# Kernel optimization log

Hardware: AMD Instinct MI355X
Metric: run time of the kernel (lower is better)

The kernel has to match this reference:

```python
import jax, jax.numpy as jnp
import numpy as np

B, NUM_ENT, NEI, NUM_REL, S, D, TOPK = 256, 100000, 128, 5000, 32, 128, 64


def setup_inputs() -> dict:
    key = jax.random.key(0)
    ks = jax.random.split(key, 9)
    return {
        "query_head": jax.random.randint(ks[0], (B,), 0, NUM_ENT, dtype=jnp.int32),
        "edge_matrix": jax.random.randint(ks[1], (NUM_ENT, NEI, 2), 0, NUM_REL, dtype=jnp.int32),
        "support_rel_all": jax.random.randint(ks[2], (S,), 0, NUM_REL, dtype=jnp.int32),
        "cos_rel_all": jax.random.normal(ks[3], (NUM_REL, NUM_REL), dtype=jnp.float32),
        "rel_emb": jax.random.normal(ks[4], (NUM_REL, D), dtype=jnp.float32) * 0.02,
        "W_ih": jax.random.normal(ks[5], (3 * D, D), dtype=jnp.float32) * 0.05,
        "W_hh": jax.random.normal(ks[6], (3 * D, D), dtype=jnp.float32) * 0.05,
        "b_ih": jax.random.normal(ks[7], (3 * D,), dtype=jnp.float32) * 0.05,
        "b_hh": jax.random.normal(ks[8], (3 * D,), dtype=jnp.float32) * 0.05,
    }


def gru_cell(x, h, W_ih, W_hh, b_ih, b_hh):
    # torch.nn.GRUCell math. x, h: [..., D]
    gi = x @ W_ih.T + b_ih
    gh = h @ W_hh.T + b_hh
    i_r, i_z, i_n = jnp.split(gi, 3, axis=-1)
    h_r, h_z, h_n = jnp.split(gh, 3, axis=-1)
    r = jax.nn.sigmoid(i_r + h_r)
    z = jax.nn.sigmoid(i_z + h_z)
    n = jnp.tanh(i_n + r * h_n)
    return (1.0 - z) * n + z * h


def reference(query_head, edge_matrix, support_rel_all, cos_rel_all, rel_emb,
              W_ih, W_hh, b_ih, b_hh):
    b = query_head.shape[0]
    nei = edge_matrix.shape[1]
    d = rel_emb.shape[1]
    sub = cos_rel_all[support_rel_all]  # [S, num_rel]

    def expand(cur):  # cur: [b, C] int entity ids
        cand = edge_matrix[cur]                       # [b, C, nei, 2]
        cand_ent, cand_rel = cand[..., 0], cand[..., 1]
        # max over support relations of cos similarity: [b, C, nei]
        score = jnp.max(sub[:, cand_rel], axis=0)
        flat = score.reshape(b, -1)                   # [b, C*nei]
        k = min(TOPK, flat.shape[-1])
        _, idx = jax.lax.top_k(flat, k)               # [b, k]
        parent = idx // nei                           # [b, k]
        aim_ent = jnp.take_along_axis(cand_ent.reshape(b, -1), idx, axis=1)
        aim_rel = jnp.take_along_axis(cand_rel.reshape(b, -1), idx, axis=1)
        return aim_ent, aim_rel, parent

    # step 1 (root -> level 1), hidden starts at zero
    e1, r1, _ = expand(query_head[:, None])
    k = e1.shape[1]
    h1 = gru_cell(rel_emb[r1], jnp.zeros((b, k, d), rel_emb.dtype), W_ih, W_hh, b_ih, b_hh)

    # step 2
    e2, r2, p2 = expand(e1)
    parent_emb2 = jnp.take_along_axis(h1, p2[..., None], axis=1)
    parent_node2 = jnp.take_along_axis(e1, p2, axis=1)
    rel1_at2 = jnp.take_along_axis(r1, p2, axis=1)
    h2 = gru_cell(rel_emb[r2], parent_emb2, W_ih, W_hh, b_ih, b_hh)

    # step 3
    e3, r3, p3 = expand(e2)
    parent_emb3 = jnp.take_along_axis(h2, p3[..., None], axis=1)
    parent_node3 = jnp.take_along_axis(e2, p3, axis=1)
    rel2_at3 = jnp.take_along_axis(r2, p3, axis=1)
    h3 = gru_cell(rel_emb[r3], parent_emb3, W_ih, W_hh, b_ih, b_hh)

    f32 = jnp.float32
    tree_node = jnp.stack([e1, e2, e3], axis=1)                    # [b, 3, k]
    tree_emb_all = jnp.stack([h1, h2, h3], axis=1)                 # [b, 3, k, d]
    parent_index = jnp.stack(
        [p2.astype(f32), p3.astype(f32),
         jnp.broadcast_to(jnp.arange(k, dtype=f32), (b, k))], axis=1)
    parent_node = jnp.stack(
        [jnp.broadcast_to(query_head[:, None], (b, k)), parent_node2, parent_node3], axis=1)
    aim_rel_all = jnp.stack([rel1_at2, rel2_at3, r3], axis=1)
    return tree_node, tree_emb_all, parent_index, parent_node, aim_rel_all
```

## Files before the change

### kernel.cpp

```cpp
#include <hip/hip_runtime.h>
#include <hip/hip_bf16.h>

#define NEI     128
#define NUM_REL 5000
#define NSUP    32
#define D       128
#define K_TOP   64
#define NB      256
#define ROWSZ   (K_TOP * D)

#define TN_OFF  0
#define TE_OFF  49152
#define PI_OFF  6340608
#define PN_OFF  6389760
#define AR_OFF  6438912

#define SENT 0xFFFFFFFFu

typedef __hip_bfloat16 bf16;
__device__ __forceinline__ float frbf(bf16 b) { return __bfloat162float(b); }
__device__ __forceinline__ float b2f(unsigned short u) {
    unsigned x = ((unsigned)u) << 16;
    return __uint_as_float(x);
}
__device__ __forceinline__ unsigned umin2(unsigned a, unsigned b) { return a < b ? a : b; }

__device__ __forceinline__ float ldin(const void* p, size_t idx, bool isbf) {
    return isbf ? frbf(((const bf16*)p)[idx]) : ((const float*)p)[idx];
}

__device__ __forceinline__ void detect_bf16(const void* probe, int tid, int* s_flag) {
    if (tid < 64) {
        unsigned w = ((const unsigned*)probe)[tid];
        unsigned e = (w >> 7) & 0xFFu;
        unsigned long long m = __ballot(e >= 100 && e <= 135);
        if (tid == 0) *s_flag = (__popcll(m) >= 48) ? 1 : 0;
    }
    __syncthreads();
}

__device__ __forceinline__ void gemm_8x8(const float* hs, const void* W,
                                         bool isbf, int gi_, int gj,
                                         float acc[8][8]) {
    if (!isbf) {
        const float* Wf = (const float*)W;
        #pragma unroll 2
        for (int kt = 0; kt < D; kt += 4) {
            float4 hv[8], wv[8];
            #pragma unroll
            for (int n = 0; n < 8; n++)
                wv[n] = *(const float4*)&Wf[(size_t)(gj + 48 * n) * D + kt];
            #pragma unroll
            for (int m = 0; m < 8; m++)
                hv[m] = *(const float4*)&hs[(gi_ + 8 * m) * 132 + kt];
            #pragma unroll
            for (int m = 0; m < 8; m++)
                #pragma unroll
                for (int n = 0; n < 8; n++)
                    acc[m][n] += hv[m].x * wv[n].x + hv[m].y * wv[n].y
                               + hv[m].z * wv[n].z + hv[m].w * wv[n].w;
        }
    } else {
        const ushort* Wb = (const ushort*)W;
        #pragma unroll 2
        for (int kt = 0; kt < D; kt += 4) {
            float4 hv[8], wv[8];
            #pragma unroll
            for (int n = 0; n < 8; n++) {
                ushort4 t = *(const ushort4*)&Wb[(size_t)(gj + 48 * n) * D + kt];
                wv[n].x = b2f(t.x); wv[n].y = b2f(t.y);
                wv[n].z = b2f(t.z); wv[n].w = b2f(t.w);
            }
            #pragma unroll
            for (int m = 0; m < 8; m++)
                hv[m] = *(const float4*)&hs[(gi_ + 8 * m) * 132 + kt];
            #pragma unroll
            for (int m = 0; m < 8; m++)
                #pragma unroll
                for (int n = 0; n < 8; n++)
                    acc[m][n] += hv[m].x * wv[n].x + hv[m].y * wv[n].y
                               + hv[m].z * wv[n].z + hv[m].w * wv[n].w;
        }
    }
}

__global__ __launch_bounds__(256) void k_rank(const int* __restrict__ support,
                                              const void* __restrict__ cosm,
                                              int* __restrict__ rnk) {
    __shared__ float ms[NUM_REL];
    __shared__ int sup[NSUP];
    __shared__ int s_isbf;
    const int tid = threadIdx.x;
    detect_bf16(cosm, tid, &s_isbf);
    const bool isbf = (bool)s_isbf;
    if (tid < NSUP) sup[tid] = support[tid];
    __syncthreads();
    for (int i = tid; i < NUM_REL; i += 256) {
        float m = -INFINITY;
        #pragma unroll
        for (int s = 0; s < NSUP; s++)
            m = fmaxf(m, ldin(cosm, (size_t)sup[s] * NUM_REL + i, isbf));
        ms[i] = m;
    }
    __syncthreads();
    int r = blockIdx.x * 256 + tid;
    if (r < NUM_REL) {
        float mine = ms[r];
        int c = 0;
        for (int i = 0; i < NUM_REL; i++) c += (ms[i] > mine);
        rnk[r] = c;
    }
}

__global__ __launch_bounds__(256) void k_expand1(
    const int* __restrict__ query, const int* __restrict__ edge,
    const int* __restrict__ rnk, float* __restrict__ out)
{
    __shared__ unsigned keys[NEI];
    __shared__ int2 pairs[NEI];
    const int tid = threadIdx.x;
    const int b = blockIdx.x;
    const int q = query[b];

    if (tid < NEI) {
        int2 pr = ((const int2*)edge)[(size_t)q * NEI + tid];
        pairs[tid] = pr;
        keys[tid] = ((unsigned)rnk[pr.y] << 13) | (unsigned)tid;
    }
    for (int size = 2; size <= NEI; size <<= 1) {
        for (int stride = size >> 1; stride > 0; stride >>= 1) {
            __syncthreads();
            if (tid < NEI) {
                int partner = tid ^ stride;
                if (partner > tid) {
                    unsigned a = keys[tid], c2 = keys[partner];
                    bool asc = ((tid & size) == 0);
                    if (asc ? (a > c2) : (a < c2)) { keys[tid] = c2; keys[partner] = a; }
                }
            }
        }
    }
    __syncthreads();
    if (tid < K_TOP) {
        int idx = keys[tid] & 8191;
        int2 p = pairs[idx];
        float* su = out + TE_OFF + ((size_t)b * 3 + 1) * ROWSZ;
        su[tid]         = (float)p.x;
        su[K_TOP + tid] = (float)p.y;
        out[TN_OFF + (b * 3 + 0) * K_TOP + tid] = (float)p.x;
        out[PN_OFF + (b * 3 + 0) * K_TOP + tid] = (float)q;
        out[PI_OFF + (b * 3 + 2) * K_TOP + tid] = (float)tid;
    }
}

__global__ __launch_bounds__(384) void k_expand(
    const int* __restrict__ edge, const int* __restrict__ rnk,
    float* __restrict__ out, const int level)
{
    __shared__ int pe[K_TOP], prl[K_TOP];
    __shared__ unsigned topks[K_TOP];
    __shared__ unsigned wred[6];

    const int tid = threadIdx.x;
    const int b = blockIdx.x;
    const int2* edge2 = (const int2*)edge;

    if (tid < K_TOP) {
        const float* su = out + TE_OFF + ((size_t)b * 3 + (level - 1)) * ROWSZ;
        pe[tid]  = (int)su[tid];
        prl[tid] = (int)su[K_TOP + tid];
    }
    __syncthreads();

    unsigned kreg[22];
    #pragma unroll
    for (int i = 0; i < 22; i++) {
        int j = tid + i * 384;
        unsigned k = SENT;
        if (j < K_TOP * NEI) {
            int rel = edge2[(size_t)pe[j >> 7] * NEI + (j & 127)].y;
            k = ((unsigned)rnk[rel] << 13) | (unsigned)j;
        }
        kreg[i] = k;
    }
    unsigned lmin = SENT;
    #pragma unroll
    for (int i = 0; i < 22; i++) lmin = umin2(lmin, kreg[i]);

    const int wid = tid >> 6;
    for (int it = 0; it < K_TOP; it++) {
        unsigned m = lmin;
        #pragma unroll
        for (int off = 32; off > 0; off >>= 1)
            m = umin2(m, (unsigned)__shfl_xor((int)m, off, 64));
        if ((tid & 63) == 0) wred[wid] = m;
        __syncthreads();
        unsigned g = umin2(umin2(umin2(wred[0], wred[1]), umin2(wred[2], wred[3])),
                           umin2(wred[4], wred[5]));
        if (tid == 0) topks[it] = g;
        if (lmin == g) {
            unsigned nl = SENT;
            #pragma unroll
            for (int i = 0; i < 22; i++) {
                if (kreg[i] == g) kreg[i] = SENT;
                nl = umin2(nl, kreg[i]);
            }
            lmin = nl;
        }
        __syncthreads();
    }

    if (tid < K_TOP) {
        int j = topks[tid] & 8191;
        int p = j >> 7, t = j & 127;
        int2 pr2 = edge2[(size_t)pe[p] * NEI + t];
        const int L1 = level - 1;
        out[TN_OFF + (b * 3 + L1) * K_TOP + tid]          = (float)pr2.x;
        out[PI_OFF + (b * 3 + (level - 2)) * K_TOP + tid] = (float)p;
        out[PN_OFF + (b * 3 + L1) * K_TOP + tid]          = (float)pe[p];
        out[AR_OFF + (b * 3 + (level - 2)) * K_TOP + tid] = (float)prl[p];
        if (level == 3)
            out[AR_OFF + (b * 3 + 2) * K_TOP + tid]       = (float)pr2.y;
        if (level == 2) {
            float* su = out + TE_OFF + ((size_t)b * 3 + 2) * ROWSZ;
            su[tid]         = (float)pr2.x;
            su[K_TOP + tid] = (float)pr2.y;
        }
    }
}

__global__ __launch_bounds__(384) void k_gru(
    const void* __restrict__ rel_emb,
    const void* __restrict__ W_ih, const void* __restrict__ b_ih,
    const void* __restrict__ W_hh, const void* __restrict__ b_hh,
    float* __restrict__ out, const void* __restrict__ cosm, const int level)
{
    extern __shared__ char smem[];
    float* hs   = (float*)smem;
    float* bufA = (float*)(smem + 33792);
    float* bufB = (float*)(smem + 33792 + 12320);

    __shared__ int selr[K_TOP], selp[K_TOP];
    __shared__ int s_isbf;

    const int tid = threadIdx.x;
    const int b   = blockIdx.x;

    detect_bf16(cosm, tid, &s_isbf);
    const bool isbf = (bool)s_isbf;

    if (tid < K_TOP) {
        size_t rbase;
        if (level == 1)      rbase = TE_OFF + ((size_t)b * 3 + 1) * ROWSZ + K_TOP;
        else if (level == 2) rbase = TE_OFF + ((size_t)b * 3 + 2) * ROWSZ + K_TOP;
        else                 rbase = AR_OFF + ((size_t)b * 3 + 2) * K_TOP;
        selr[tid] = (int)out[rbase + tid];
        if (level >= 2) {
            size_t pbase = PI_OFF + ((size_t)b * 3 + (level - 2)) * K_TOP;
            selp[tid] = (int)out[pbase + tid];
        }
    }
    __syncthreads();

    const int gi_ = tid & 7;
    const int gj  = tid >> 3;

    for (int idx = tid; idx < K_TOP * D; idx += 384) {
        int i = idx >> 7, d = idx & 127;
        hs[i * 132 + d] = ldin(rel_emb, (size_t)selr[i] * D + d, isbf);
    }
    __syncthreads();

    float accA[8][8];
    #pragma unroll
    for (int m = 0; m < 8; m++)
        #pragma unroll
        for (int n = 0; n < 8; n++) accA[m][n] = 0.f;
    gemm_8x8(hs, W_ih, isbf, gi_, gj, accA);

    float accB[8][8];
    #pragma unroll
    for (int m = 0; m < 8; m++)
        #pragma unroll
        for (int n = 0; n < 8; n++) accB[m][n] = 0.f;

    if (level >= 2) {
        __syncthreads();
        const float* hrow = out + TE_OFF + ((size_t)b * 3 + (level - 2)) * ROWSZ;
        for (int idx = tid; idx < K_TOP * D; idx += 384) {
            int i = idx >> 7, d = idx & 127;
            hs[i * 132 + d] = hrow[selp[i] * D + d];
        }
        __syncthreads();
        gemm_8x8(hs, W_hh, isbf, gi_, gj, accB);
    }

    float bih[8];
    #pragma unroll
    for (int n = 0; n < 8; n++) bih[n] = ldin(b_ih, gj + 48 * n, isbf);

    for (int c = 0; c < 8; c++) {
        __syncthreads();
        #pragma unroll
        for (int n = 0; n < 8; n++) {
            bufA[gi_ * 385 + gj + 48 * n] = accA[c][n] + bih[n];
            bufB[gi_ * 385 + gj + 48 * n] = (level >= 2) ? accB[c][n] : 0.f;
        }
        __syncthreads();
        for (int idx = tid; idx < 8 * D; idx += 384) {
            int iloc = idx >> 7, d = idx & 127;
            int node = 8 * c + iloc;
            float i_r = bufA[iloc * 385 + d];
            float i_z = bufA[iloc * 385 + 128 + d];
            float i_n = bufA[iloc * 385 + 256 + d];
            float h_r = bufB[iloc * 385 + d] + ldin(b_hh, d, isbf);
            float h_z = bufB[iloc * 385 + 128 + d] + ldin(b_hh, D + d, isbf);
            float h_n = bufB[iloc * 385 + 256 + d] + ldin(b_hh, 2 * D + d, isbf);
            float rg = 1.f / (1.f + expf(-(i_r + h_r)));
            float z  = 1.f / (1.f + expf(-(i_z + h_z)));
            float nn = tanhf(i_n + rg * h_n);
            float hprev = (level >= 2) ? hs[node * 132 + d] : 0.f;
            out[TE_OFF + ((size_t)b * 3 + (level - 1)) * ROWSZ + node * D + d]
                = (1.f - z) * nn + z * hprev;
        }
    }
}

extern "C" void kernel_launch(void* const* d_in, const int* in_sizes, int n_in,
                              void* d_out, int out_size, void* d_ws, size_t ws_size,
                              hipStream_t stream)
{
    const int*  query   = (const int*)d_in[0];
    const int*  edge    = (const int*)d_in[1];
    const int*  support = (const int*)d_in[2];
    const void* cosm    = d_in[3];
    const void* rel_emb = d_in[4];
    const void* W_ih    = d_in[5];
    const void* W_hh    = d_in[6];
    const void* b_ih    = d_in[7];
    const void* b_hh    = d_in[8];
    float* out = (float*)d_out;

    int* rnk = (int*)d_ws;

    k_rank<<<(NUM_REL + 255) / 256, 256, 0, stream>>>(support, cosm, rnk);
    k_expand1<<<NB, 256, 0, stream>>>(query, edge, rnk, out);
    k_gru<<<NB, 384, 58432, stream>>>(rel_emb, W_ih, b_ih, W_hh, b_hh,
                                      out, cosm, 1);
    k_expand<<<NB, 384, 0, stream>>>(edge, rnk, out, 2);
    k_gru<<<NB, 384, 58432, stream>>>(rel_emb, W_ih, b_ih, W_hh, b_hh,
                                      out, cosm, 2);
    k_expand<<<NB, 384, 0, stream>>>(edge, rnk, out, 3);
    k_gru<<<NB, 384, 58432, stream>>>(rel_emb, W_ih, b_ih, W_hh, b_hh,
                                      out, cosm, 3);
}
```

Before: 623.0 us.

## Stage bf16 GRU weights in LDS, vectorize rank kernel, cache b_hh in shared

Adds a bf16 GEMM path that stages 96-row weight slices into shared memory in four passes, instead of reading weights from global memory per thread. Vectorizes the support-max and rank-count loops in k_rank with float4/ushort4 loads. Preloads b_hh into shared memory so the GRU epilogue avoids repeated global loads. The tiled path adds extra barriers and a larger dynamic shared allocation.

```diff
diff --git a/kernel.cpp b/kernel.cpp
--- a/kernel.cpp
+++ b/kernel.cpp
@@ -39,55 +39,63 @@
     __syncthreads();
 }
 
-__device__ __forceinline__ void gemm_8x8(const float* hs, const void* W,
-                                         bool isbf, int gi_, int gj,
-                                         float acc[8][8]) {
-    if (!isbf) {
-        const float* Wf = (const float*)W;
+__device__ __forceinline__ void gemm_tiled_bf16(const float* hs, char* wq,
+                                                const ushort* Wb, int tid,
+                                                int gi_, int gj, float acc[8][8]) {
+    for (int q = 0; q < 4; q++) {
+        __syncthreads();
+        const uint4* Wg = (const uint4*)(Wb + (size_t)96 * q * D);
+        for (int t = tid; t < 1536; t += 384) {
+            int row = t >> 4, c = t & 15;
+            *(uint4*)(wq + row * 272 + c * 16) = Wg[row * 16 + c];
+        }
+        __syncthreads();
+        const int n0 = 2 * q;
         #pragma unroll 2
         for (int kt = 0; kt < D; kt += 4) {
-            float4 hv[8], wv[8];
-            #pragma unroll
-            for (int n = 0; n < 8; n++)
-                wv[n] = *(const float4*)&Wf[(size_t)(gj + 48 * n) * D + kt];
+            ushort4 t0 = *(const ushort4*)(wq + gj * 272 + kt * 2);
+            ushort4 t1 = *(const ushort4*)(wq + (gj + 48) * 272 + kt * 2);
+            float4 wv0 = make_float4(b2f(t0.x), b2f(t0.y), b2f(t0.z), b2f(t0.w));
+            float4 wv1 = make_float4(b2f(t1.x), b2f(t1.y), b2f(t1.z), b2f(t1.w));
+            float4 hv[8];
             #pragma unroll
             for (int m = 0; m < 8; m++)
                 hv[m] = *(const float4*)&hs[(gi_ + 8 * m) * 132 + kt];
             #pragma unroll
-            for (int m = 0; m < 8; m++)
-                #pragma unroll
-                for (int n = 0; n < 8; n++)
-                    acc[m][n] += hv[m].x * wv[n].x + hv[m].y * wv[n].y
-                               + hv[m].z * wv[n].z + hv[m].w * wv[n].w;
-        }
-    } else {
-        const ushort* Wb = (const ushort*)W;
-        #pragma unroll 2
-        for (int kt = 0; kt < D; kt += 4) {
-            float4 hv[8], wv[8];
-            #pragma unroll
-            for (int n = 0; n < 8; n++) {
-                ushort4 t = *(const ushort4*)&Wb[(size_t)(gj + 48 * n) * D + kt];
-                wv[n].x = b2f(t.x); wv[n].y = b2f(t.y);
-                wv[n].z = b2f(t.z); wv[n].w = b2f(t.w);
-            }
-            #pragma unroll
-            for (int m = 0; m < 8; m++)
-                hv[m] = *(const float4*)&hs[(gi_ + 8 * m) * 132 + kt];
-            #pragma unroll
-            for (int m = 0; m < 8; m++)
-                #pragma unroll
-                for (int n = 0; n < 8; n++)
-                    acc[m][n] += hv[m].x * wv[n].x + hv[m].y * wv[n].y
-                               + hv[m].z * wv[n].z + hv[m].w * wv[n].w;
-        }
+            for (int m = 0; m < 8; m++) {
+                acc[m][n0]     += hv[m].x * wv0.x + hv[m].y * wv0.y
+                                + hv[m].z * wv0.z + hv[m].w * wv0.w;
+                acc[m][n0 + 1] += hv[m].x * wv1.x + hv[m].y * wv1.y
+                                + hv[m].z * wv1.z + hv[m].w * wv1.w;
+            }
+        }
+    }
+}
+
+__device__ __forceinline__ void gemm_glob_f32(const float* hs, const float* Wf,
+                                              int gi_, int gj, float acc[8][8]) {
+    #pragma unroll 2
+    for (int kt = 0; kt < D; kt += 4) {
+        float4 hv[8], wv[8];
+        #pragma unroll
+        for (int n = 0; n < 8; n++)
+            wv[n] = *(const float4*)&Wf[(size_t)(gj + 48 * n) * D + kt];
+        #pragma unroll
+        for (int m = 0; m < 8; m++)
+            hv[m] = *(const float4*)&hs[(gi_ + 8 * m) * 132 + kt];
+        #pragma unroll
+        for (int m = 0; m < 8; m++)
+            #pragma unroll
+            for (int n = 0; n < 8; n++)
+                acc[m][n] += hv[m].x * wv[n].x + hv[m].y * wv[n].y
+                           + hv[m].z * wv[n].z + hv[m].w * wv[n].w;
     }
 }
 
 __global__ __launch_bounds__(256) void k_rank(const int* __restrict__ support,
                                               const void* __restrict__ cosm,
                                               int* __restrict__ rnk) {
-    __shared__ float ms[NUM_REL];
+    __shared__ __align__(16) float ms[NUM_REL];
     __shared__ int sup[NSUP];
     __shared__ int s_isbf;
     const int tid = threadIdx.x;
@@ -95,19 +103,44 @@
     const bool isbf = (bool)s_isbf;
     if (tid < NSUP) sup[tid] = support[tid];
     __syncthreads();
-    for (int i = tid; i < NUM_REL; i += 256) {
-        float m = -INFINITY;
-        #pragma unroll
-        for (int s = 0; s < NSUP; s++)
-            m = fmaxf(m, ldin(cosm, (size_t)sup[s] * NUM_REL + i, isbf));
-        ms[i] = m;
-    }
-    __syncthreads();
+
+    float4* ms4 = (float4*)ms;
+    const int NC4 = NUM_REL / 4;
+    if (!isbf) {
+        const float* cf = (const float*)cosm;
+        for (int i4 = tid; i4 < NC4; i4 += 256) {
+            float4 m = make_float4(-INFINITY, -INFINITY, -INFINITY, -INFINITY);
+            #pragma unroll
+            for (int s = 0; s < NSUP; s++) {
+                float4 v = *(const float4*)&cf[(size_t)sup[s] * NUM_REL + i4 * 4];
+                m.x = fmaxf(m.x, v.x); m.y = fmaxf(m.y, v.y);
+                m.z = fmaxf(m.z, v.z); m.w = fmaxf(m.w, v.w);
+            }
+            ms4[i4] = m;
+        }
+    } else {
+        const ushort* cb = (const ushort*)cosm;
+        for (int i4 = tid; i4 < NC4; i4 += 256) {
+            float4 m = make_float4(-INFINITY, -INFINITY, -INFINITY, -INFINITY);
+            #pragma unroll
+            for (int s = 0; s < NSUP; s++) {
+                ushort4 t = *(const ushort4*)&cb[(size_t)sup[s] * NUM_REL + i4 * 4];
+                m.x = fmaxf(m.x, b2f(t.x)); m.y = fmaxf(m.y, b2f(t.y));
+                m.z = fmaxf(m.z, b2f(t.z)); m.w = fmaxf(m.w, b2f(t.w));
+            }
+            ms4[i4] = m;
+        }
+    }
+    __syncthreads();
+
     int r = blockIdx.x * 256 + tid;
     if (r < NUM_REL) {
         float mine = ms[r];
         int c = 0;
-        for (int i = 0; i < NUM_REL; i++) c += (ms[i] > mine);
+        for (int i4 = 0; i4 < NC4; i4++) {
+            float4 v = ms4[i4];
+            c += (v.x > mine) + (v.y > mine) + (v.z > mine) + (v.w > mine);
+        }
         rnk[r] = c;
     }
 }
@@ -237,10 +270,12 @@
 {
     extern __shared__ char smem[];
     float* hs   = (float*)smem;
+    char*  wq   = smem + 33792;
     float* bufA = (float*)(smem + 33792);
     float* bufB = (float*)(smem + 33792 + 12320);
 
     __shared__ int selr[K_TOP], selp[K_TOP];
+    __shared__ float sbhh[3 * D];
     __shared__ int s_isbf;
 
     const int tid = threadIdx.x;
@@ -260,6 +295,7 @@
             selp[tid] = (int)out[pbase + tid];
         }
     }
+    if (tid < 3 * D) sbhh[tid] = ldin(b_hh, tid, isbf);
     __syncthreads();
 
     const int gi_ = tid & 7;
@@ -276,7 +312,8 @@
     for (int m = 0; m < 8; m++)
         #pragma unroll
         for (int n = 0; n < 8; n++) accA[m][n] = 0.f;
-    gemm_8x8(hs, W_ih, isbf, gi_, gj, accA);
+    if (isbf) gemm_tiled_bf16(hs, wq, (const ushort*)W_ih, tid, gi_, gj, accA);
+    else      gemm_glob_f32(hs, (const float*)W_ih, gi_, gj, accA);
 
     float accB[8][8];
     #pragma unroll
@@ -292,7 +329,8 @@
             hs[i * 132 + d] = hrow[selp[i] * D + d];
         }
         __syncthreads();
-        gemm_8x8(hs, W_hh, isbf, gi_, gj, accB);
+        if (isbf) gemm_tiled_bf16(hs, wq, (const ushort*)W_hh, tid, gi_, gj, accB);
+        else      gemm_glob_f32(hs, (const float*)W_hh, gi_, gj, accB);
     }
 
     float bih[8];
@@ -313,9 +351,9 @@
             float i_r = bufA[iloc * 385 + d];
             float i_z = bufA[iloc * 385 + 128 + d];
             float i_n = bufA[iloc * 385 + 256 + d];
-            float h_r = bufB[iloc * 385 + d] + ldin(b_hh, d, isbf);
-            float h_z = bufB[iloc * 385 + 128 + d] + ldin(b_hh, D + d, isbf);
-            float h_n = bufB[iloc * 385 + 256 + d] + ldin(b_hh, 2 * D + d, isbf);
+            float h_r = bufB[iloc * 385 + d] + sbhh[d];
+            float h_z = bufB[iloc * 385 + 128 + d] + sbhh[D + d];
+            float h_n = bufB[iloc * 385 + 256 + d] + sbhh[2 * D + d];
             float rg = 1.f / (1.f + expf(-(i_r + h_r)));
             float z  = 1.f / (1.f + expf(-(i_z + h_z)));
             float nn = tanhf(i_n + rg * h_n);
@@ -345,12 +383,12 @@
 
     k_rank<<<(NUM_REL + 255) / 256, 256, 0, stream>>>(support, cosm, rnk);
     k_expand1<<<NB, 256, 0, stream>>>(query, edge, rnk, out);
-    k_gru<<<NB, 384, 58432, stream>>>(rel_emb, W_ih, b_ih, W_hh, b_hh,
+    k_gru<<<NB, 384, 59904, stream>>>(rel_emb, W_ih, b_ih, W_hh, b_hh,
                                       out, cosm, 1);
     k_expand<<<NB, 384, 0, stream>>>(edge, rnk, out, 2);
-    k_gru<<<NB, 384, 58432, stream>>>(rel_emb, W_ih, b_ih, W_hh, b_hh,
+    k_gru<<<NB, 384, 59904, stream>>>(rel_emb, W_ih, b_ih, W_hh, b_hh,
                                       out, cosm, 2);
     k_expand<<<NB, 384, 0, stream>>>(edge, rnk, out, 3);
-    k_gru<<<NB, 384, 58432, stream>>>(rel_emb, W_ih, b_ih, W_hh, b_hh,
+    k_gru<<<NB, 384, 59904, stream>>>(rel_emb, W_ih, b_ih, W_hh, b_hh,
                                       out, cosm, 3);
 }
```

Result: no change. 622.2 us (-0.1%).
